# Optimization experiments

Measured on AMD Instinct MI355X. Metric: run time of the kernel, lower is better.

The kernel has to match this reference:

```python
import jax, jax.numpy as jnp
import numpy as np

B, T, S = 32, 64, 64
V, E, H, L = 32000, 512, 512, 2


def setup_inputs() -> dict:
    key = jax.random.key(0)
    ks = jax.random.split(key, 20)
    sc = 0.02
    inp = {
        "target_input": jax.random.randint(ks[0], (B, T), 0, V),
        "target_mask": jnp.ones((B, T), dtype=bool),
        "enc_outs": jax.random.normal(ks[1], (B, S, H), dtype=jnp.float32),
        "h0": jax.random.normal(ks[2], (L, B, H), dtype=jnp.float32) * 0.1,
        "c0": jax.random.normal(ks[3], (L, B, H), dtype=jnp.float32) * 0.1,
        "source_mask": jnp.ones((B, S), dtype=bool),
    }
    emb = jax.random.normal(ks[4], (V, E), dtype=jnp.float32) * sc
    inp["emb"] = emb.at[0].set(0.0)  # padding_idx = 0
    # LSTM layer 0: input = emb + context = E + H
    inp["W_ih0"] = jax.random.normal(ks[5], (4 * H, E + H), dtype=jnp.float32) * sc
    inp["W_hh0"] = jax.random.normal(ks[6], (4 * H, H), dtype=jnp.float32) * sc
    inp["b_ih0"] = jnp.zeros((4 * H,), dtype=jnp.float32)
    inp["b_hh0"] = jnp.zeros((4 * H,), dtype=jnp.float32)
    # LSTM layer 1: input = H
    inp["W_ih1"] = jax.random.normal(ks[7], (4 * H, H), dtype=jnp.float32) * sc
    inp["W_hh1"] = jax.random.normal(ks[8], (4 * H, H), dtype=jnp.float32) * sc
    inp["b_ih1"] = jnp.zeros((4 * H,), dtype=jnp.float32)
    inp["b_hh1"] = jnp.zeros((4 * H,), dtype=jnp.float32)
    # output projection: (hid + hid + emb) -> vocab
    inp["fc_W"] = jax.random.normal(ks[9], (V, 2 * H + E), dtype=jnp.float32) * sc
    inp["fc_b"] = jnp.zeros((V,), dtype=jnp.float32)
    return inp


def _lstm_cell(x, h, c, W_ih, W_hh, b_ih, b_hh):
    g = x @ W_ih.T + h @ W_hh.T + b_ih + b_hh  # (B, 4H)
    i, f, gg, o = jnp.split(g, 4, axis=-1)  # PyTorch gate order i,f,g,o
    c_new = jax.nn.sigmoid(f) * c + jax.nn.sigmoid(i) * jnp.tanh(gg)
    h_new = jax.nn.sigmoid(o) * jnp.tanh(c_new)
    return h_new, c_new


def reference(target_input, target_mask, enc_outs, h0, c0, source_mask,
              emb, W_ih0, W_hh0, b_ih0, b_hh0, W_ih1, W_hh1, b_ih1, b_hh1,
              fc_W, fc_b):
    inv_sqrt_h = 1.0 / jnp.sqrt(jnp.asarray(H, dtype=enc_outs.dtype))
    layers = ((W_ih0, W_hh0, b_ih0, b_hh0), (W_ih1, W_hh1, b_ih1, b_hh1))

    def step(carry, tok):
        h, c = carry  # each (L, B, H)
        emb_t = emb[tok]  # (B, E)
        q = h[-1]  # (B, H)
        scores = jnp.einsum('bh,bsh->bs', q, enc_outs) * inv_sqrt_h
        scores = jnp.where(source_mask, scores, jnp.asarray(-1e9, scores.dtype))
        attn = jax.nn.softmax(scores, axis=-1)  # (B, S)
        ctx = jnp.einsum('bs,bsh->bh', attn, enc_outs)  # (B, H)
        x = jnp.concatenate([emb_t, ctx], axis=-1)  # (B, E+H)
        hs, cs = [], []
        for l, (W_ih, W_hh, b_ih, b_hh) in enumerate(layers):
            hl, cl = _lstm_cell(x, h[l], c[l], W_ih, W_hh, b_ih, b_hh)
            hs.append(hl); cs.append(cl)
            x = hl
        h_new = jnp.stack(hs)
        c_new = jnp.stack(cs)
        concat = jnp.concatenate([hs[-1], ctx, emb_t], axis=-1)  # (B, 2H+E)
        logit = concat @ fc_W.T + fc_b  # (B, V)
        return (h_new, c_new), (logit, attn)

    tokens = target_input.T  # (T, B)
    (h, c), (logits, attns) = jax.lax.scan(step, (h0, c0), tokens)
    outputs = jnp.transpose(logits, (1, 0, 2))       # (B, T, V)
    attn_weights = jnp.transpose(attns, (1, 0, 2))   # (B, T, S)
    return outputs, h, c, attn_weights
```

## Files before the change

kernel.cpp:

```cpp
#include <hip/hip_runtime.h>
#include <hip/hip_bf16.h>
#include <cstddef>

#define BB 32
#define TT 64
#define SS 64
#define VV 32000
#define EE 512
#define HH 512
#define CAT 1536
#define ROWS 2048

#define OUT_LOGITS 0
#define OUT_H   ((size_t)ROWS * VV)
#define OUT_C   (OUT_H + 2 * BB * HH)
#define OUT_ATTN (OUT_C + 2 * BB * HH)

typedef __attribute__((ext_vector_type(8))) __bf16 bf16x8;
typedef __attribute__((ext_vector_type(4))) float f32x4;

__global__ __launch_bounds__(128) void k_embed(const int* __restrict__ tok,
                                               const float* __restrict__ emb,
                                               float* __restrict__ cat) {
    int row = blockIdx.x;
    int tid = threadIdx.x;
    int tk = tok[row];
    const float4* src = (const float4*)(emb + (size_t)tk * EE);
    float4* dst = (float4*)(cat + (size_t)row * CAT + 1024);
    dst[tid] = src[tid];
}

__global__ __launch_bounds__(256) void k_attn(const float* __restrict__ h1prev,
                                              const float* __restrict__ enc,
                                              float* __restrict__ cat,
                                              float* __restrict__ attn_out,
                                              int t) {
    int b = blockIdx.x;
    int tid = threadIdx.x;
    int lane = tid & 63;
    int w = tid >> 6;

    __shared__ float q[HH];
    __shared__ float at[SS];
    __shared__ float sc[SS];

    for (int i = tid; i < HH; i += 256) q[i] = h1prev[b * HH + i];
    __syncthreads();

    const float* encb = enc + (size_t)b * SS * HH;

    for (int i = 0; i < 16; ++i) {
        int s = w * 16 + i;
        const float* er = encb + s * HH;
        float acc = 0.f;
        #pragma unroll
        for (int j = 0; j < 8; ++j) acc += q[lane * 8 + j] * er[lane * 8 + j];
        #pragma unroll
        for (int off = 32; off > 0; off >>= 1) acc += __shfl_xor(acc, off);
        if (lane == 0) sc[s] = acc * 0.044194173824159216f;
    }
    __syncthreads();

    if (w == 0) {
        float v = sc[lane];
        float m = v;
        #pragma unroll
        for (int off = 32; off > 0; off >>= 1) m = fmaxf(m, __shfl_xor(m, off));
        float e = expf(v - m);
        float sum = e;
        #pragma unroll
        for (int off = 32; off > 0; off >>= 1) sum += __shfl_xor(sum, off);
        float a = e / sum;
        at[lane] = a;
        attn_out[((size_t)b * TT + t) * SS + lane] = a;
    }
    __syncthreads();

    int h0i = tid * 2;
    float c0 = 0.f, c1 = 0.f;
    for (int s = 0; s < SS; ++s) {
        float a = at[s];
        c0 += a * encb[s * HH + h0i];
        c1 += a * encb[s * HH + h0i + 1];
    }
    float* dst = cat + ((size_t)b * TT + t) * CAT + 512;
    dst[h0i] = c0;
    dst[h0i + 1] = c1;
}

template <int LAYER>
__global__ __launch_bounds__(256) void k_lstm(const float* __restrict__ cat,
                                              const float* __restrict__ hprev,
                                              const float* __restrict__ xh,
                                              const float* __restrict__ cprev,
                                              float* __restrict__ hnew,
                                              float* __restrict__ cnew,
                                              float* __restrict__ cat_h1,
                                              const float* __restrict__ Wih,
                                              const float* __restrict__ Whh,
                                              const float* __restrict__ bih,
                                              const float* __restrict__ bhh,
                                              int t) {
    constexpr int KIH = (LAYER == 0) ? 1024 : 512;
    constexpr int KTOT = KIH + 512;
    constexpr int NCH = KTOT / 64;

    int tid = threadIdx.x;
    int lane = tid & 63;
    int w = tid >> 6;
    int hbase = blockIdx.x * 2;

    __shared__ float xs[32][64];
    __shared__ float gs[2][4][32];

    float accA[32], accB[32];
    #pragma unroll
    for (int b = 0; b < 32; ++b) { accA[b] = 0.f; accB[b] = 0.f; }

    int jA = w * 512 + hbase;
    int jB = jA + 1;

    int lb = tid >> 3;
    int lk = (tid & 7) * 8;

    for (int ch = 0; ch < NCH; ++ch) {
        int k0 = ch * 64;
        const float* src;
        if (LAYER == 0) {
            if (k0 < 512)       src = cat + ((size_t)(lb * TT + t)) * CAT + 1024 + k0;
            else if (k0 < 1024) src = cat + ((size_t)(lb * TT + t)) * CAT + k0;
            else                src = hprev + lb * HH + (k0 - 1024);
        } else {
            if (k0 < 512)       src = xh + lb * HH + k0;
            else                src = hprev + lb * HH + (k0 - 512);
        }
        __syncthreads();
        float4 v0 = *(const float4*)(src + lk);
        float4 v1 = *(const float4*)(src + lk + 4);
        *(float4*)&xs[lb][lk] = v0;
        *(float4*)&xs[lb][lk + 4] = v1;
        __syncthreads();

        const float *wA, *wB;
        if (k0 < KIH) {
            wA = Wih + (size_t)jA * KIH + k0;
            wB = Wih + (size_t)jB * KIH + k0;
        } else {
            wA = Whh + (size_t)jA * 512 + (k0 - KIH);
            wB = Whh + (size_t)jB * 512 + (k0 - KIH);
        }
        float wva = wA[lane];
        float wvb = wB[lane];
        #pragma unroll
        for (int b = 0; b < 32; ++b) {
            float xv = xs[b][lane];
            accA[b] = fmaf(xv, wva, accA[b]);
            accB[b] = fmaf(xv, wvb, accB[b]);
        }
    }

    #pragma unroll
    for (int b = 0; b < 32; ++b) {
        float a = accA[b], bb = accB[b];
        #pragma unroll
        for (int off = 32; off > 0; off >>= 1) {
            a += __shfl_xor(a, off);
            bb += __shfl_xor(bb, off);
        }
        if (lane == b) { gs[0][w][b] = a; gs[1][w][b] = bb; }
    }
    __syncthreads();

    if (tid < 64) {
        int hl = tid >> 5;
        int b = tid & 31;
        int hg = hbase + hl;
        float gi = gs[hl][0][b] + bih[0 * 512 + hg] + bhh[0 * 512 + hg];
        float gf = gs[hl][1][b] + bih[1 * 512 + hg] + bhh[1 * 512 + hg];
        float gg = gs[hl][2][b] + bih[2 * 512 + hg] + bhh[2 * 512 + hg];
        float go = gs[hl][3][b] + bih[3 * 512 + hg] + bhh[3 * 512 + hg];
        float si = 1.f / (1.f + expf(-gi));
        float sf = 1.f / (1.f + expf(-gf));
        float so = 1.f / (1.f + expf(-go));
        float tg = tanhf(gg);
        float cp = cprev[b * HH + hg];
        float cn = sf * cp + si * tg;
        float hn = so * tanhf(cn);
        cnew[b * HH + hg] = cn;
        hnew[b * HH + hg] = hn;
        if (LAYER == 1) cat_h1[((size_t)(b * TT + t)) * CAT + hg] = hn;
    }
}

#define FBK 32
#define LDP 40

__device__ __forceinline__ void split8(const float* __restrict__ s,
                                       bf16x8& h, bf16x8& l) {
    #pragma unroll
    for (int j = 0; j < 8; ++j) {
        float x = s[j];
        __bf16 hb = (__bf16)x;
        h[j] = hb;
        l[j] = (__bf16)(x - (float)hb);
    }
}

__global__ __launch_bounds__(256) void k_fc_mfma(const float* __restrict__ cat,
                                                 const float* __restrict__ W,
                                                 const float* __restrict__ bias,
                                                 float* __restrict__ out) {
    __shared__ __attribute__((aligned(16))) __bf16 Ahi[128][LDP];
    __shared__ __attribute__((aligned(16))) __bf16 Alo[128][LDP];
    __shared__ __attribute__((aligned(16))) __bf16 Bhi[128][LDP];
    __shared__ __attribute__((aligned(16))) __bf16 Blo[128][LDP];

    int bn = blockIdx.x;
    int bm = blockIdx.y;
    int tid = threadIdx.x;
    int lane = tid & 63;
    int wid = tid >> 6;
    int wm = (wid >> 1) * 64;
    int wn = (wid & 1) * 64;
    int lr = lane & 15;
    int lk = (lane >> 4) * 8;

    int sm = tid >> 1;
    int sk = (tid & 1) * 16;

    const float* aRow = cat + (size_t)(bm * 128 + sm) * CAT + sk;
    const float* bRow = W + (size_t)(bn * 128 + sm) * CAT + sk;

    f32x4 acc[4][4];
    #pragma unroll
    for (int i = 0; i < 4; ++i)
        #pragma unroll
        for (int j = 0; j < 4; ++j) acc[i][j] = (f32x4)(0.f);

    for (int k0 = 0; k0 < CAT; k0 += FBK) {
        float ta[16], tb[16];
        {
            const float4* ap = (const float4*)(aRow + k0);
            const float4* bp = (const float4*)(bRow + k0);
            float4* tap = (float4*)ta;
            float4* tbp = (float4*)tb;
            #pragma unroll
            for (int i = 0; i < 4; ++i) { tap[i] = ap[i]; tbp[i] = bp[i]; }
        }
        bf16x8 h0, l0, h1, l1, h2, l2, h3, l3;
        split8(ta, h0, l0); split8(ta + 8, h1, l1);
        split8(tb, h2, l2); split8(tb + 8, h3, l3);

        __syncthreads();
        *(bf16x8*)&Ahi[sm][sk]     = h0;
        *(bf16x8*)&Ahi[sm][sk + 8] = h1;
        *(bf16x8*)&Alo[sm][sk]     = l0;
        *(bf16x8*)&Alo[sm][sk + 8] = l1;
        *(bf16x8*)&Bhi[sm][sk]     = h2;
        *(bf16x8*)&Bhi[sm][sk + 8] = h3;
        *(bf16x8*)&Blo[sm][sk]     = l2;
        *(bf16x8*)&Blo[sm][sk + 8] = l3;
        __syncthreads();

        bf16x8 ah[4], al[4];
        #pragma unroll
        for (int mi = 0; mi < 4; ++mi) {
            ah[mi] = *(const bf16x8*)&Ahi[wm + mi * 16 + lr][lk];
            al[mi] = *(const bf16x8*)&Alo[wm + mi * 16 + lr][lk];
        }
        #pragma unroll
        for (int ni = 0; ni < 4; ++ni) {
            bf16x8 bh = *(const bf16x8*)&Bhi[wn + ni * 16 + lr][lk];
            bf16x8 bl = *(const bf16x8*)&Blo[wn + ni * 16 + lr][lk];
            #pragma unroll
            for (int mi = 0; mi < 4; ++mi) {
                acc[mi][ni] = __builtin_amdgcn_mfma_f32_16x16x32_bf16(ah[mi], bh, acc[mi][ni], 0, 0, 0);
                acc[mi][ni] = __builtin_amdgcn_mfma_f32_16x16x32_bf16(ah[mi], bl, acc[mi][ni], 0, 0, 0);
                acc[mi][ni] = __builtin_amdgcn_mfma_f32_16x16x32_bf16(al[mi], bh, acc[mi][ni], 0, 0, 0);
            }
        }
    }

    int row0 = bm * 128 + wm + (lane >> 4) * 4;
    int col0 = bn * 128 + wn + lr;
    #pragma unroll
    for (int ni = 0; ni < 4; ++ni) {
        int col = col0 + ni * 16;
        float bv = bias[col];
        #pragma unroll
        for (int mi = 0; mi < 4; ++mi) {
            int row = row0 + mi * 16;
            #pragma unroll
            for (int r = 0; r < 4; ++r) {
                out[(size_t)(row + r) * VV + col] = acc[mi][ni][r] + bv;
            }
        }
    }
}

extern "C" void kernel_launch(void* const* d_in, const int* in_sizes, int n_in,
                              void* d_out, int out_size, void* d_ws, size_t ws_size,
                              hipStream_t stream) {
    const int*   tgt  = (const int*)d_in[0];
    const float* enc  = (const float*)d_in[2];
    const float* h0   = (const float*)d_in[3];
    const float* c0   = (const float*)d_in[4];
    const float* emb  = (const float*)d_in[6];
    const float* Wih0 = (const float*)d_in[7];
    const float* Whh0 = (const float*)d_in[8];
    const float* bih0 = (const float*)d_in[9];
    const float* bhh0 = (const float*)d_in[10];
    const float* Wih1 = (const float*)d_in[11];
    const float* Whh1 = (const float*)d_in[12];
    const float* bih1 = (const float*)d_in[13];
    const float* bhh1 = (const float*)d_in[14];
    const float* fcW  = (const float*)d_in[15];
    const float* fcb  = (const float*)d_in[16];

    float* out = (float*)d_out;
    float* ws  = (float*)d_ws;

    float* cat = ws;
    float* hs  = ws + (size_t)ROWS * CAT;
    float* cs  = hs + 4 * BB * HH;

    const size_t stateBytes = (size_t)2 * BB * HH * sizeof(float);

    hipMemcpyAsync(hs, h0, stateBytes, hipMemcpyDeviceToDevice, stream);
    hipMemcpyAsync(cs, c0, stateBytes, hipMemcpyDeviceToDevice, stream);

    k_embed<<<ROWS, 128, 0, stream>>>(tgt, emb, cat);

    for (int t = 0; t < TT; ++t) {
        int rb = t & 1;
        int wb = 1 - rb;
        float* h_r = hs + (size_t)rb * 2 * BB * HH;
        float* h_w = hs + (size_t)wb * 2 * BB * HH;
        float* c_r = cs + (size_t)rb * 2 * BB * HH;
        float* c_w = cs + (size_t)wb * 2 * BB * HH;

        k_attn<<<BB, 256, 0, stream>>>(h_r + BB * HH, enc, cat, out + OUT_ATTN, t);

        k_lstm<0><<<256, 256, 0, stream>>>(cat, h_r, nullptr, c_r,
                                           h_w, c_w, nullptr,
                                           Wih0, Whh0, bih0, bhh0, t);

        k_lstm<1><<<256, 256, 0, stream>>>(cat, h_r + BB * HH, h_w, c_r + BB * HH,
                                           h_w + BB * HH, c_w + BB * HH, cat,
                                           Wih1, Whh1, bih1, bhh1, t);
    }

    hipMemcpyAsync(out + OUT_H, hs, stateBytes, hipMemcpyDeviceToDevice, stream);
    hipMemcpyAsync(out + OUT_C, cs, stateBytes, hipMemcpyDeviceToDevice, stream);

    k_fc_mfma<<<dim3(VV / 128, ROWS / 128), 256, 0, stream>>>(cat, fcW, fcb, out);
}
```

Measured before the change: 5.766 ms.

## Fuse recurrent loop into one persistent kernel with grid barriers

Replaces the 192 per-step kernel launches (attention, LSTM layer 0, LSTM layer 1) with a single persistent kernel of 256 blocks. The blocks step through time and synchronise with an atomic grid barrier held in workspace memory. This removes launch overhead and inter-kernel gaps on the sequential critical path, at the cost of spin-wait barriers and a dependence on all 256 blocks being co-resident. It also swaps the FC GEMM grid axes so that consecutive blocks walk the row tiles for a given weight tile, which may improve weight reuse in cache.

```diff
diff --git a/kernel.cpp b/kernel.cpp
--- a/kernel.cpp
+++ b/kernel.cpp
@@ -10,6 +10,7 @@
 #define HH 512
 #define CAT 1536
 #define ROWS 2048
+#define NBLK 256
 
 #define OUT_LOGITS 0
 #define OUT_H   ((size_t)ROWS * VV)
@@ -30,88 +31,47 @@
     dst[tid] = src[tid];
 }
 
-__global__ __launch_bounds__(256) void k_attn(const float* __restrict__ h1prev,
-                                              const float* __restrict__ enc,
-                                              float* __restrict__ cat,
-                                              float* __restrict__ attn_out,
-                                              int t) {
-    int b = blockIdx.x;
-    int tid = threadIdx.x;
-    int lane = tid & 63;
-    int w = tid >> 6;
-
-    __shared__ float q[HH];
-    __shared__ float at[SS];
-    __shared__ float sc[SS];
-
-    for (int i = tid; i < HH; i += 256) q[i] = h1prev[b * HH + i];
+__device__ __forceinline__ void grid_barrier(unsigned* bar) {
     __syncthreads();
-
-    const float* encb = enc + (size_t)b * SS * HH;
-
-    for (int i = 0; i < 16; ++i) {
-        int s = w * 16 + i;
-        const float* er = encb + s * HH;
-        float acc = 0.f;
-        #pragma unroll
-        for (int j = 0; j < 8; ++j) acc += q[lane * 8 + j] * er[lane * 8 + j];
-        #pragma unroll
-        for (int off = 32; off > 0; off >>= 1) acc += __shfl_xor(acc, off);
-        if (lane == 0) sc[s] = acc * 0.044194173824159216f;
+    if (threadIdx.x == 0) {
+        __threadfence();
+        unsigned g = __hip_atomic_load(&bar[1], __ATOMIC_ACQUIRE, __HIP_MEMORY_SCOPE_AGENT);
+        unsigned a = __hip_atomic_fetch_add(&bar[0], 1u, __ATOMIC_ACQ_REL, __HIP_MEMORY_SCOPE_AGENT);
+        if (a == NBLK - 1u) {
+            __hip_atomic_store(&bar[0], 0u, __ATOMIC_RELAXED, __HIP_MEMORY_SCOPE_AGENT);
+            __hip_atomic_fetch_add(&bar[1], 1u, __ATOMIC_ACQ_REL, __HIP_MEMORY_SCOPE_AGENT);
+        } else {
+            while (__hip_atomic_load(&bar[1], __ATOMIC_ACQUIRE, __HIP_MEMORY_SCOPE_AGENT) == g) {
+                __builtin_amdgcn_s_sleep(1);
+            }
+        }
+        __threadfence();
     }
     __syncthreads();
-
-    if (w == 0) {
-        float v = sc[lane];
-        float m = v;
-        #pragma unroll
-        for (int off = 32; off > 0; off >>= 1) m = fmaxf(m, __shfl_xor(m, off));
-        float e = expf(v - m);
-        float sum = e;
-        #pragma unroll
-        for (int off = 32; off > 0; off >>= 1) sum += __shfl_xor(sum, off);
-        float a = e / sum;
-        at[lane] = a;
-        attn_out[((size_t)b * TT + t) * SS + lane] = a;
-    }
-    __syncthreads();
-
-    int h0i = tid * 2;
-    float c0 = 0.f, c1 = 0.f;
-    for (int s = 0; s < SS; ++s) {
-        float a = at[s];
-        c0 += a * encb[s * HH + h0i];
-        c1 += a * encb[s * HH + h0i + 1];
-    }
-    float* dst = cat + ((size_t)b * TT + t) * CAT + 512;
-    dst[h0i] = c0;
-    dst[h0i + 1] = c1;
 }
 
 template <int LAYER>
-__global__ __launch_bounds__(256) void k_lstm(const float* __restrict__ cat,
-                                              const float* __restrict__ hprev,
-                                              const float* __restrict__ xh,
-                                              const float* __restrict__ cprev,
-                                              float* __restrict__ hnew,
-                                              float* __restrict__ cnew,
-                                              float* __restrict__ cat_h1,
-                                              const float* __restrict__ Wih,
-                                              const float* __restrict__ Whh,
-                                              const float* __restrict__ bih,
-                                              const float* __restrict__ bhh,
-                                              int t) {
+__device__ __forceinline__ void lstm_phase(int blk, int tid, int t,
+                                           const float* __restrict__ cat,
+                                           const float* __restrict__ hprev,
+                                           const float* __restrict__ xh,
+                                           const float* __restrict__ cprev,
+                                           float* __restrict__ hnew,
+                                           float* __restrict__ cnew,
+                                           float* __restrict__ cat_h1,
+                                           const float* __restrict__ Wih,
+                                           const float* __restrict__ Whh,
+                                           const float* __restrict__ bih,
+                                           const float* __restrict__ bhh,
+                                           float (&xs)[32][64],
+                                           float (&gs)[2][4][32]) {
     constexpr int KIH = (LAYER == 0) ? 1024 : 512;
     constexpr int KTOT = KIH + 512;
     constexpr int NCH = KTOT / 64;
 
-    int tid = threadIdx.x;
     int lane = tid & 63;
     int w = tid >> 6;
-    int hbase = blockIdx.x * 2;
-
-    __shared__ float xs[32][64];
-    __shared__ float gs[2][4][32];
+    int hbase = blk * 2;
 
     float accA[32], accB[32];
     #pragma unroll
@@ -192,6 +152,99 @@
     }
 }
 
+__global__ __launch_bounds__(256) void k_recur(float* __restrict__ cat,
+                                               float* __restrict__ hs,
+                                               float* __restrict__ cs,
+                                               const float* __restrict__ enc,
+                                               float* __restrict__ attn_out,
+                                               unsigned* __restrict__ bar,
+                                               const float* __restrict__ Wih0,
+                                               const float* __restrict__ Whh0,
+                                               const float* __restrict__ bih0,
+                                               const float* __restrict__ bhh0,
+                                               const float* __restrict__ Wih1,
+                                               const float* __restrict__ Whh1,
+                                               const float* __restrict__ bih1,
+                                               const float* __restrict__ bhh1) {
+    int tid = threadIdx.x;
+    int lane = tid & 63;
+    int w = tid >> 6;
+    int blk = blockIdx.x;
+
+    __shared__ float q[HH];
+    __shared__ float sc[SS];
+    __shared__ float at[SS];
+    __shared__ float xs[32][64];
+    __shared__ float gs[2][4][32];
+
+    for (int t = 0; t < TT; ++t) {
+        int rb = t & 1;
+        int wb = 1 - rb;
+        float* h_r = hs + (size_t)rb * 2 * BB * HH;
+        float* h_w = hs + (size_t)wb * 2 * BB * HH;
+        float* c_r = cs + (size_t)rb * 2 * BB * HH;
+        float* c_w = cs + (size_t)wb * 2 * BB * HH;
+
+        if (blk < BB) {
+            int b = blk;
+            const float* h1prev = h_r + BB * HH;
+            for (int i = tid; i < HH; i += 256) q[i] = h1prev[b * HH + i];
+            __syncthreads();
+
+            const float* encb = enc + (size_t)b * SS * HH;
+
+            for (int i = 0; i < 16; ++i) {
+                int s = w * 16 + i;
+                const float* er = encb + s * HH;
+                float acc = 0.f;
+                #pragma unroll
+                for (int j = 0; j < 8; ++j) acc += q[lane * 8 + j] * er[lane * 8 + j];
+                #pragma unroll
+                for (int off = 32; off > 0; off >>= 1) acc += __shfl_xor(acc, off);
+                if (lane == 0) sc[s] = acc * 0.044194173824159216f;
+            }
+            __syncthreads();
+
+            if (w == 0) {
+                float v = sc[lane];
+                float m = v;
+                #pragma unroll
+                for (int off = 32; off > 0; off >>= 1) m = fmaxf(m, __shfl_xor(m, off));
+                float e = expf(v - m);
+                float sum = e;
+                #pragma unroll
+                for (int off = 32; off > 0; off >>= 1) sum += __shfl_xor(sum, off);
+                float a = e / sum;
+                at[lane] = a;
+                attn_out[((size_t)b * TT + t) * SS + lane] = a;
+            }
+            __syncthreads();
+
+            int h0i = tid * 2;
+            float cc0 = 0.f, cc1 = 0.f;
+            for (int s = 0; s < SS; ++s) {
+                float a = at[s];
+                cc0 += a * encb[s * HH + h0i];
+                cc1 += a * encb[s * HH + h0i + 1];
+            }
+            float* dst = cat + ((size_t)b * TT + t) * CAT + 512;
+            dst[h0i] = cc0;
+            dst[h0i + 1] = cc1;
+        }
+        grid_barrier(bar);
+
+        lstm_phase<0>(blk, tid, t, cat, h_r, nullptr, c_r,
+                      h_w, c_w, nullptr,
+                      Wih0, Whh0, bih0, bhh0, xs, gs);
+        grid_barrier(bar);
+
+        lstm_phase<1>(blk, tid, t, cat, h_r + BB * HH, h_w, c_r + BB * HH,
+                      h_w + BB * HH, c_w + BB * HH, cat,
+                      Wih1, Whh1, bih1, bhh1, xs, gs);
+        grid_barrier(bar);
+    }
+}
+
 #define FBK 32
 #define LDP 40
 
@@ -215,8 +268,8 @@
     __shared__ __attribute__((aligned(16))) __bf16 Bhi[128][LDP];
     __shared__ __attribute__((aligned(16))) __bf16 Blo[128][LDP];
 
-    int bn = blockIdx.x;
-    int bm = blockIdx.y;
+    int bm = blockIdx.x;
+    int bn = blockIdx.y;
     int tid = threadIdx.x;
     int lane = tid & 63;
     int wid = tid >> 6;
@@ -323,35 +376,23 @@
     float* cat = ws;
     float* hs  = ws + (size_t)ROWS * CAT;
     float* cs  = hs + 4 * BB * HH;
+    unsigned* bar = (unsigned*)(cs + 4 * BB * HH);
 
     const size_t stateBytes = (size_t)2 * BB * HH * sizeof(float);
+
+    hipMemsetAsync(bar, 0, 2 * sizeof(unsigned), stream);
 
     hipMemcpyAsync(hs, h0, stateBytes, hipMemcpyDeviceToDevice, stream);
     hipMemcpyAsync(cs, c0, stateBytes, hipMemcpyDeviceToDevice, stream);
 
     k_embed<<<ROWS, 128, 0, stream>>>(tgt, emb, cat);
 
-    for (int t = 0; t < TT; ++t) {
-        int rb = t & 1;
-        int wb = 1 - rb;
-        float* h_r = hs + (size_t)rb * 2 * BB * HH;
-        float* h_w = hs + (size_t)wb * 2 * BB * HH;
-        float* c_r = cs + (size_t)rb * 2 * BB * HH;
-        float* c_w = cs + (size_t)wb * 2 * BB * HH;
-
-        k_attn<<<BB, 256, 0, stream>>>(h_r + BB * HH, enc, cat, out + OUT_ATTN, t);
-
-        k_lstm<0><<<256, 256, 0, stream>>>(cat, h_r, nullptr, c_r,
-                                           h_w, c_w, nullptr,
-                                           Wih0, Whh0, bih0, bhh0, t);
-
-        k_lstm<1><<<256, 256, 0, stream>>>(cat, h_r + BB * HH, h_w, c_r + BB * HH,
-                                           h_w + BB * HH, c_w + BB * HH, cat,
-                                           Wih1, Whh1, bih1, bhh1, t);
-    }
+    k_recur<<<NBLK, 256, 0, stream>>>(cat, hs, cs, enc, out + OUT_ATTN, bar,
+                                      Wih0, Whh0, bih0, bhh0,
+                                      Wih1, Whh1, bih1, bhh1);
 
     hipMemcpyAsync(out + OUT_H, hs, stateBytes, hipMemcpyDeviceToDevice, stream);
     hipMemcpyAsync(out + OUT_C, cs, stateBytes, hipMemcpyDeviceToDevice, stream);
 
-    k_fc_mfma<<<dim3(VV / 128, ROWS / 128), 256, 0, stream>>>(cat, fcW, fcb, out);
-}
+    k_fc_mfma<<<dim3(ROWS / 128, VV / 128), 256, 0, stream>>>(cat, fcW, fcb, out);
+}
```

New measurement: 17.44 ms. 3.02x slower.
